# Kernel optimization log

Hardware: AMD Instinct MI355X
Metric: run time of the kernel (lower is better)

## Reference

```python
import jax, jax.numpy as jnp
import numpy as np

N_NODES = 50000
N_EDGES = 200000
IN_FEATS = 32
OUT_FEATS = 32
EDGE_DIM = 16


def setup_inputs() -> dict:
    key = jax.random.key(0)
    k1, k2, k3, k4, k5 = jax.random.split(key, 5)
    feat = jax.random.normal(k1, (N_NODES, IN_FEATS), dtype=jnp.float32)
    efeat = jax.random.normal(k2, (N_EDGES, EDGE_DIM), dtype=jnp.float32)
    src = jax.random.randint(k3, (N_EDGES,), 0, N_NODES, dtype=jnp.int32)
    dst = jax.random.randint(k4, (N_EDGES,), 0, N_NODES, dtype=jnp.int32)
    # edge_func = Linear(EDGE_DIM -> IN_FEATS*OUT_FEATS)
    W_edge = jax.random.normal(k5, (EDGE_DIM, IN_FEATS * OUT_FEATS), dtype=jnp.float32) * (1.0 / np.sqrt(EDGE_DIM))
    b_edge = jnp.zeros((IN_FEATS * OUT_FEATS,), dtype=jnp.float32)
    bias = jnp.zeros((OUT_FEATS,), dtype=jnp.float32)
    return {"feat": feat, "efeat": efeat, "src": src, "dst": dst,
            "W_edge": W_edge, "b_edge": b_edge, "bias": bias}


def reference(feat, efeat, src, dst, W_edge, b_edge, bias):
    # edge_func: (E, edge_dim) -> (E, in, out) edge-conditioned weights
    w = (efeat @ W_edge + b_edge).reshape(-1, IN_FEATS, OUT_FEATS)
    # u_mul_e + sum over in dim  ==  per-edge matvec: h_src[e] @ W[e]
    h_src = feat[src]                               # (E, in) gather
    msg = jnp.einsum('ei,eio->eo', h_src, w)        # (E, out)
    # mean reduce over incoming edges per destination node
    agg = jax.ops.segment_sum(msg, dst, num_segments=N_NODES)   # (N, out)
    deg = jax.ops.segment_sum(jnp.ones((msg.shape[0],), dtype=msg.dtype), dst,
                              num_segments=N_NODES)
    agg = agg / jnp.maximum(deg, 1.0)[:, None]      # zero-degree nodes stay 0
    return agg + bias
```

## Files before the change

kernel.cpp:

```cpp
#include <hip/hip_runtime.h>
#include <hip/hip_bf16.h>

#define NNODES 50000
#define NEDGES 200000
#define WCT_ROW 552
#define WCT_BYTES (32 * WCT_ROW * 2)
#define HROW 40
#define TILE_EDGES 64
#define NTILES (NEDGES / TILE_EDGES)
#define CHAIN_BLKS ((NEDGES + 255) / 256)
#define DROW 36

#define MSG_OFF   0
#define HEAD_OFF  25600000
#define NEXT_OFF  25800000
#define WCT_OFF   26600000

using f32x4 = __attribute__((ext_vector_type(4))) float;
using f16x2 = __attribute__((ext_vector_type(2))) _Float16;
using f16x4 = __attribute__((ext_vector_type(4))) _Float16;
using f16x8 = __attribute__((ext_vector_type(8))) _Float16;

__device__ __forceinline__ f16x2 pkrtz(float a, float b) {
    return __builtin_bit_cast(f16x2, __builtin_amdgcn_cvt_pkrtz(a, b));
}

__device__ __forceinline__ void gload_lds16(const void* g, void* l) {
    __builtin_amdgcn_global_load_lds(
        (const __attribute__((address_space(1))) unsigned int*)g,
        (__attribute__((address_space(3))) unsigned int*)l, 16, 0, 0);
}

#define WCT_BLKS 69
__global__ void init_kernel(const float* __restrict__ W_edge,
                            const float* __restrict__ b_edge,
                            _Float16* __restrict__ wct,
                            unsigned* __restrict__ head) {
    int b = blockIdx.x;
    if (b < WCT_BLKS) {
        int gid = b * 256 + threadIdx.x;
        if (gid >= 32 * WCT_ROW) return;
        int n = gid / WCT_ROW;
        int c = gid - n * WCT_ROW;
        float v = 0.0f;
        if (c < 512)      v = W_edge[(c & 15) * 1024 + (c >> 4) * 32 + n];
        else if (c < 544) v = b_edge[(c - 512) * 32 + n];
        wct[gid] = (_Float16)v;
    } else {
        int gid = (b - WCT_BLKS) * 256 + threadIdx.x;
        if (gid < NNODES) head[gid] = 0xFFFFFFFFu;
    }
}

__global__ __launch_bounds__(256, 3) void work_kernel(
    const float* __restrict__ feat, const float* __restrict__ efeat,
    const int* __restrict__ src, const int* __restrict__ dst,
    const _Float16* __restrict__ wct_g,
    float4* __restrict__ msg4, unsigned* __restrict__ head,
    unsigned* __restrict__ next) {

    __shared__ __align__(16) unsigned short wct_lds[32 * WCT_ROW];
    __shared__ __align__(16) unsigned short h_lds[TILE_EDGES * HROW];
    __shared__ __align__(16) float dtile[TILE_EDGES * DROW];

    const int t = threadIdx.x;

    if (blockIdx.x >= NTILES) {
        int e = (blockIdx.x - NTILES) * 256 + t;
        if (e < NEDGES)
            next[e] = atomicExch(&head[dst[e]], (unsigned)e);
        return;
    }

    const int lane = t & 63;
    const int wave = t >> 6;
    const int ebase = blockIdx.x * TILE_EDGES;

    {
        const char* gsrc = (const char*)wct_g;
        char* lbase = (char*)wct_lds;
        #pragma unroll
        for (int c = 0; c < 9; ++c) {
            int chunk = wave + c * 4;
            if (chunk < 35) {
                int boff = (chunk << 10) + lane * 16;
                if (boff < WCT_BYTES) gload_lds16(gsrc + boff, lbase + boff);
            }
        }
    }

    {
        int et = t >> 2, p = t & 3;
        int se = src[ebase + et];
        const float* fp = feat + se * 32 + p * 8;
        float4 a = *(const float4*)fp;
        float4 b = *(const float4*)(fp + 4);
        uint4 hp;
        hp.x = __builtin_bit_cast(unsigned int, pkrtz(a.x, a.y));
        hp.y = __builtin_bit_cast(unsigned int, pkrtz(a.z, a.w));
        hp.z = __builtin_bit_cast(unsigned int, pkrtz(b.x, b.y));
        hp.w = __builtin_bit_cast(unsigned int, pkrtz(b.z, b.w));
        *(uint4*)(void*)(h_lds + et * HROW + p * 8) = hp;
    }

    const int r16 = lane & 15;
    const int g   = lane >> 4;
    const int wbase = wave * 16;
    const int eg = ebase + wbase + r16;

    const float* efp = efeat + eg * 16 + (g & 1) * 8;
    float4 e0 = *(const float4*)efp;
    float4 e1 = *(const float4*)(efp + 4);
    f16x2 ef2[4] = { pkrtz(e0.x, e0.y), pkrtz(e0.z, e0.w),
                     pkrtz(e1.x, e1.y), pkrtz(e1.z, e1.w) };

    __syncthreads();

    unsigned int hbc[16];
    f16x8 af_bias;
    {
        const uint4* hrow = (const uint4*)(void*)(h_lds + (wbase + r16) * HROW);
        unsigned int hw[16];
        #pragma unroll
        for (int q = 0; q < 4; ++q) {
            uint4 v = hrow[q];
            hw[q*4+0] = v.x; hw[q*4+1] = v.y; hw[q*4+2] = v.z; hw[q*4+3] = v.w;
        }
        const bool hi = (g >> 1) & 1;
        #pragma unroll
        for (int s = 0; s < 16; ++s) {
            unsigned int x = hi ? (hw[s] >> 16) : (hw[s] & 0xffffu);
            hbc[s] = x | (x << 16);
        }
        af_bias = *(const f16x8*)(void*)((const _Float16*)h_lds + (wbase + r16) * HROW + g * 8);
    }

    const _Float16* brow0 = (const _Float16*)wct_lds + r16 * WCT_ROW;
    const _Float16* brow1 = (const _Float16*)wct_lds + (16 + r16) * WCT_ROW;

    f32x4 acc0 = {0.f, 0.f, 0.f, 0.f};
    f32x4 acc1 = {0.f, 0.f, 0.f, 0.f};

    #pragma unroll
    for (int s = 0; s < 16; ++s) {
        const int koff = s * 32 + g * 8;
        f16x8 b0 = *(const f16x8*)(brow0 + koff);
        f16x8 b1 = *(const f16x8*)(brow1 + koff);
        f16x2 hb = __builtin_bit_cast(f16x2, hbc[s]);
        f16x2 p0 = hb * ef2[0], p1 = hb * ef2[1], p2 = hb * ef2[2], p3 = hb * ef2[3];
        f16x4 lo  = __builtin_shufflevector(p0, p1, 0, 1, 2, 3);
        f16x4 hi4 = __builtin_shufflevector(p2, p3, 0, 1, 2, 3);
        f16x8 af  = __builtin_shufflevector(lo, hi4, 0, 1, 2, 3, 4, 5, 6, 7);
        acc0 = __builtin_amdgcn_mfma_f32_16x16x32_f16(af, b0, acc0, 0, 0, 0);
        acc1 = __builtin_amdgcn_mfma_f32_16x16x32_f16(af, b1, acc1, 0, 0, 0);
    }
    {
        const int koff = 512 + g * 8;
        f16x8 b0 = *(const f16x8*)(brow0 + koff);
        f16x8 b1 = *(const f16x8*)(brow1 + koff);
        acc0 = __builtin_amdgcn_mfma_f32_16x16x32_f16(af_bias, b0, acc0, 0, 0, 0);
        acc1 = __builtin_amdgcn_mfma_f32_16x16x32_f16(af_bias, b1, acc1, 0, 0, 0);
    }

    {
        const int browD = wbase + g * 4;
        #pragma unroll
        for (int r = 0; r < 4; ++r) {
            dtile[(browD + r) * DROW + r16]      = acc0[r];
            dtile[(browD + r) * DROW + 16 + r16] = acc1[r];
        }
    }
    __syncthreads();

    {
        const int et = t >> 2, q = t & 3;
        const float* drow = dtile + et * DROW + q * 8;
        float4 v0 = *(const float4*)(drow);
        float4 v1 = *(const float4*)(drow + 4);
        float4* mp = msg4 + (size_t)blockIdx.x * 512;
        mp[t]       = v0;
        mp[256 + t] = v1;
    }
}

__global__ __launch_bounds__(256) void pull_kernel(
    const float4* __restrict__ msg4, const unsigned* __restrict__ head,
    const unsigned* __restrict__ next, const float* __restrict__ bias,
    float* __restrict__ out) {

    int gid = blockIdx.x * 256 + threadIdx.x;
    if (gid >= NNODES * 8) return;
    int n = gid >> 3, Q = gid & 7;

    const unsigned qoff = (unsigned)((Q & 1) * 256 + (Q >> 1));

    float4 s = {0.f, 0.f, 0.f, 0.f};
    float degf = 0.0f;

    unsigned e = head[n];
    while (e != 0xFFFFFFFFu) {
        float4 m = msg4[(size_t)(e >> 6) * 512 + qoff + (e & 63) * 4];
        s.x += m.x; s.y += m.y; s.z += m.z; s.w += m.w;
        degf += 1.0f;
        e = next[e];
    }

    float inv = 1.0f / fmaxf(degf, 1.0f);
    float4 b = ((const float4*)bias)[Q];
    float4 o = { s.x * inv + b.x, s.y * inv + b.y, s.z * inv + b.z, s.w * inv + b.w };
    *(float4*)(out + n * 32 + Q * 4) = o;
}

extern "C" void kernel_launch(void* const* d_in, const int* in_sizes, int n_in,
                              void* d_out, int out_size, void* d_ws, size_t ws_size,
                              hipStream_t stream) {
    const float* feat   = (const float*)d_in[0];
    const float* efeat  = (const float*)d_in[1];
    const int*   src    = (const int*)d_in[2];
    const int*   dst    = (const int*)d_in[3];
    const float* W_edge = (const float*)d_in[4];
    const float* b_edge = (const float*)d_in[5];
    const float* bias   = (const float*)d_in[6];

    char* ws = (char*)d_ws;
    float4*   msg4 = (float4*)(ws + MSG_OFF);
    unsigned* head = (unsigned*)(ws + HEAD_OFF);
    unsigned* next = (unsigned*)(ws + NEXT_OFF);
    _Float16* wct  = (_Float16*)(ws + WCT_OFF);
    float*    out  = (float*)d_out;

    init_kernel<<<WCT_BLKS + (NNODES + 255) / 256, 256, 0, stream>>>(
        W_edge, b_edge, wct, head);
    work_kernel<<<NTILES + CHAIN_BLKS, 256, 0, stream>>>(
        feat, efeat, src, dst, wct, msg4, head, next);
    pull_kernel<<<(NNODES * 8 + 255) / 256, 256, 0, stream>>>(
        msg4, head, next, bias, out);
}
```

Baseline: 46.44 us.

## Read edge-weight matrix from global cache instead of staging in LDS

```diff
diff --git a/kernel.cpp b/kernel.cpp
--- a/kernel.cpp
+++ b/kernel.cpp
@@ -3,8 +3,7 @@
 
 #define NNODES 50000
 #define NEDGES 200000
-#define WCT_ROW 552
-#define WCT_BYTES (32 * WCT_ROW * 2)
+#define WCT_ROW 544
 #define HROW 40
 #define TILE_EDGES 64
 #define NTILES (NEDGES / TILE_EDGES)
@@ -25,13 +24,7 @@
     return __builtin_bit_cast(f16x2, __builtin_amdgcn_cvt_pkrtz(a, b));
 }
 
-__device__ __forceinline__ void gload_lds16(const void* g, void* l) {
-    __builtin_amdgcn_global_load_lds(
-        (const __attribute__((address_space(1))) unsigned int*)g,
-        (__attribute__((address_space(3))) unsigned int*)l, 16, 0, 0);
-}
-
-#define WCT_BLKS 69
+#define WCT_BLKS 68
 __global__ void init_kernel(const float* __restrict__ W_edge,
                             const float* __restrict__ b_edge,
                             _Float16* __restrict__ wct,
@@ -42,9 +35,9 @@
         if (gid >= 32 * WCT_ROW) return;
         int n = gid / WCT_ROW;
         int c = gid - n * WCT_ROW;
-        float v = 0.0f;
-        if (c < 512)      v = W_edge[(c & 15) * 1024 + (c >> 4) * 32 + n];
-        else if (c < 544) v = b_edge[(c - 512) * 32 + n];
+        float v;
+        if (c < 512) v = W_edge[(c & 15) * 1024 + (c >> 4) * 32 + n];
+        else         v = b_edge[(c - 512) * 32 + n];
         wct[gid] = (_Float16)v;
     } else {
         int gid = (b - WCT_BLKS) * 256 + threadIdx.x;
@@ -52,14 +45,13 @@
     }
 }
 
-__global__ __launch_bounds__(256, 3) void work_kernel(
+__global__ __launch_bounds__(256, 6) void work_kernel(
     const float* __restrict__ feat, const float* __restrict__ efeat,
     const int* __restrict__ src, const int* __restrict__ dst,
     const _Float16* __restrict__ wct_g,
     float4* __restrict__ msg4, unsigned* __restrict__ head,
     unsigned* __restrict__ next) {
 
-    __shared__ __align__(16) unsigned short wct_lds[32 * WCT_ROW];
     __shared__ __align__(16) unsigned short h_lds[TILE_EDGES * HROW];
     __shared__ __align__(16) float dtile[TILE_EDGES * DROW];
 
@@ -75,19 +67,6 @@
     const int lane = t & 63;
     const int wave = t >> 6;
     const int ebase = blockIdx.x * TILE_EDGES;
-
-    {
-        const char* gsrc = (const char*)wct_g;
-        char* lbase = (char*)wct_lds;
-        #pragma unroll
-        for (int c = 0; c < 9; ++c) {
-            int chunk = wave + c * 4;
-            if (chunk < 35) {
-                int boff = (chunk << 10) + lane * 16;
-                if (boff < WCT_BYTES) gload_lds16(gsrc + boff, lbase + boff);
-            }
-        }
-    }
 
     {
         int et = t >> 2, p = t & 3;
@@ -114,7 +93,8 @@
     f16x2 ef2[4] = { pkrtz(e0.x, e0.y), pkrtz(e0.z, e0.w),
                      pkrtz(e1.x, e1.y), pkrtz(e1.z, e1.w) };
 
-    __syncthreads();
+    asm volatile("s_waitcnt lgkmcnt(0)" ::: "memory");
+    __builtin_amdgcn_sched_barrier(0);
 
     unsigned int hbc[16];
     f16x8 af_bias;
@@ -135,8 +115,8 @@
         af_bias = *(const f16x8*)(void*)((const _Float16*)h_lds + (wbase + r16) * HROW + g * 8);
     }
 
-    const _Float16* brow0 = (const _Float16*)wct_lds + r16 * WCT_ROW;
-    const _Float16* brow1 = (const _Float16*)wct_lds + (16 + r16) * WCT_ROW;
+    const _Float16* brow0 = wct_g + r16 * WCT_ROW;
+    const _Float16* brow1 = wct_g + (16 + r16) * WCT_ROW;
 
     f32x4 acc0 = {0.f, 0.f, 0.f, 0.f};
     f32x4 acc1 = {0.f, 0.f, 0.f, 0.f};
@@ -170,7 +150,8 @@
             dtile[(browD + r) * DROW + 16 + r16] = acc1[r];
         }
     }
-    __syncthreads();
+    asm volatile("s_waitcnt lgkmcnt(0)" ::: "memory");
+    __builtin_amdgcn_sched_barrier(0);
 
     {
         const int et = t >> 2, q = t & 3;
```

Result: slower. 58.77 us (+26.5%).

## Fuse init, edge compute and pull into one persistent cooperative kernel

Applied to the files above, without the earlier changes.

```diff
diff --git a/kernel.cpp b/kernel.cpp
--- a/kernel.cpp
+++ b/kernel.cpp
@@ -1,5 +1,8 @@
 #include <hip/hip_runtime.h>
 #include <hip/hip_bf16.h>
+#include <hip/hip_cooperative_groups.h>
+
+namespace cg = cooperative_groups;
 
 #define NNODES 50000
 #define NEDGES 200000
@@ -8,8 +11,8 @@
 #define HROW 40
 #define TILE_EDGES 64
 #define NTILES (NEDGES / TILE_EDGES)
-#define CHAIN_BLKS ((NEDGES + 255) / 256)
-#define DROW 36
+#define DROW 33
+#define MAX_GRID 768
 
 #define MSG_OFF   0
 #define HEAD_OFF  25600000
@@ -31,53 +34,45 @@
         (__attribute__((address_space(3))) unsigned int*)l, 16, 0, 0);
 }
 
-#define WCT_BLKS 69
-__global__ void init_kernel(const float* __restrict__ W_edge,
-                            const float* __restrict__ b_edge,
-                            _Float16* __restrict__ wct,
-                            unsigned* __restrict__ head) {
-    int b = blockIdx.x;
-    if (b < WCT_BLKS) {
-        int gid = b * 256 + threadIdx.x;
-        if (gid >= 32 * WCT_ROW) return;
-        int n = gid / WCT_ROW;
-        int c = gid - n * WCT_ROW;
+__global__ __launch_bounds__(256, 3) void fused_kernel(
+    const float* __restrict__ feat, const float* __restrict__ efeat,
+    const int* __restrict__ src, const int* __restrict__ dst,
+    const float* __restrict__ W_edge, const float* __restrict__ b_edge,
+    const float* __restrict__ bias,
+    float4* __restrict__ msg4, unsigned* __restrict__ head,
+    unsigned* __restrict__ next, _Float16* __restrict__ wct,
+    float* __restrict__ out) {
+
+    cg::grid_group grid = cg::this_grid();
+
+    __shared__ __align__(16) unsigned short wct_lds[32 * WCT_ROW];
+    __shared__ __align__(16) unsigned short h_lds[TILE_EDGES * HROW];
+    __shared__ __align__(16) float dtile[TILE_EDGES * DROW];
+
+    const int t = threadIdx.x;
+    const int nb = gridDim.x;
+    const int gtid = blockIdx.x * 256 + t;
+    const int gstride = nb * 256;
+
+    for (int gid = gtid; gid < 32 * WCT_ROW; gid += gstride) {
+        int n = gid / WCT_ROW, c = gid - n * WCT_ROW;
         float v = 0.0f;
         if (c < 512)      v = W_edge[(c & 15) * 1024 + (c >> 4) * 32 + n];
         else if (c < 544) v = b_edge[(c - 512) * 32 + n];
         wct[gid] = (_Float16)v;
-    } else {
-        int gid = (b - WCT_BLKS) * 256 + threadIdx.x;
-        if (gid < NNODES) head[gid] = 0xFFFFFFFFu;
-    }
-}
-
-__global__ __launch_bounds__(256, 3) void work_kernel(
-    const float* __restrict__ feat, const float* __restrict__ efeat,
-    const int* __restrict__ src, const int* __restrict__ dst,
-    const _Float16* __restrict__ wct_g,
-    float4* __restrict__ msg4, unsigned* __restrict__ head,
-    unsigned* __restrict__ next) {
-
-    __shared__ __align__(16) unsigned short wct_lds[32 * WCT_ROW];
-    __shared__ __align__(16) unsigned short h_lds[TILE_EDGES * HROW];
-    __shared__ __align__(16) float dtile[TILE_EDGES * DROW];
-
-    const int t = threadIdx.x;
-
-    if (blockIdx.x >= NTILES) {
-        int e = (blockIdx.x - NTILES) * 256 + t;
-        if (e < NEDGES)
-            next[e] = atomicExch(&head[dst[e]], (unsigned)e);
-        return;
-    }
+    }
+    for (int gid = gtid; gid < NNODES; gid += gstride) head[gid] = 0xFFFFFFFFu;
+
+    grid.sync();
 
     const int lane = t & 63;
     const int wave = t >> 6;
-    const int ebase = blockIdx.x * TILE_EDGES;
+    const int r16  = lane & 15;
+    const int g    = lane >> 4;
+    const int wbase = wave * 16;
 
     {
-        const char* gsrc = (const char*)wct_g;
+        const char* gsrc = (const char*)wct;
         char* lbase = (char*)wct_lds;
         #pragma unroll
         for (int c = 0; c < 9; ++c) {
@@ -88,127 +83,126 @@
             }
         }
     }
-
-    {
-        int et = t >> 2, p = t & 3;
-        int se = src[ebase + et];
-        const float* fp = feat + se * 32 + p * 8;
-        float4 a = *(const float4*)fp;
-        float4 b = *(const float4*)(fp + 4);
-        uint4 hp;
-        hp.x = __builtin_bit_cast(unsigned int, pkrtz(a.x, a.y));
-        hp.y = __builtin_bit_cast(unsigned int, pkrtz(a.z, a.w));
-        hp.z = __builtin_bit_cast(unsigned int, pkrtz(b.x, b.y));
-        hp.w = __builtin_bit_cast(unsigned int, pkrtz(b.z, b.w));
-        *(uint4*)(void*)(h_lds + et * HROW + p * 8) = hp;
-    }
-
-    const int r16 = lane & 15;
-    const int g   = lane >> 4;
-    const int wbase = wave * 16;
-    const int eg = ebase + wbase + r16;
-
-    const float* efp = efeat + eg * 16 + (g & 1) * 8;
-    float4 e0 = *(const float4*)efp;
-    float4 e1 = *(const float4*)(efp + 4);
-    f16x2 ef2[4] = { pkrtz(e0.x, e0.y), pkrtz(e0.z, e0.w),
-                     pkrtz(e1.x, e1.y), pkrtz(e1.z, e1.w) };
-
     __syncthreads();
 
-    unsigned int hbc[16];
-    f16x8 af_bias;
-    {
-        const uint4* hrow = (const uint4*)(void*)(h_lds + (wbase + r16) * HROW);
-        unsigned int hw[16];
-        #pragma unroll
-        for (int q = 0; q < 4; ++q) {
-            uint4 v = hrow[q];
-            hw[q*4+0] = v.x; hw[q*4+1] = v.y; hw[q*4+2] = v.z; hw[q*4+3] = v.w;
-        }
-        const bool hi = (g >> 1) & 1;
+    const _Float16* brow0 = (const _Float16*)wct_lds + r16 * WCT_ROW;
+    const _Float16* brow1 = (const _Float16*)wct_lds + (16 + r16) * WCT_ROW;
+
+    for (int tile = blockIdx.x; tile < NTILES; tile += nb) {
+        const int ebase = tile * TILE_EDGES;
+
+        if (t < TILE_EDGES) {
+            int e = ebase + t;
+            next[e] = atomicExch(&head[dst[e]], (unsigned)e);
+        }
+
+        {
+            int et = t >> 2, p = t & 3;
+            int se = src[ebase + et];
+            const float* fp = feat + se * 32 + p * 8;
+            float4 a = *(const float4*)fp;
+            float4 b = *(const float4*)(fp + 4);
+            uint4 hp;
+            hp.x = __builtin_bit_cast(unsigned int, pkrtz(a.x, a.y));
+            hp.y = __builtin_bit_cast(unsigned int, pkrtz(a.z, a.w));
+            hp.z = __builtin_bit_cast(unsigned int, pkrtz(b.x, b.y));
+            hp.w = __builtin_bit_cast(unsigned int, pkrtz(b.z, b.w));
+            *(uint4*)(void*)(h_lds + et * HROW + p * 8) = hp;
+        }
+
+        const int eg = ebase + wbase + r16;
+        const float* efp = efeat + eg * 16 + (g & 1) * 8;
+        float4 e0 = *(const float4*)efp;
+        float4 e1 = *(const float4*)(efp + 4);
+        f16x2 ef2[4] = { pkrtz(e0.x, e0.y), pkrtz(e0.z, e0.w),
+                         pkrtz(e1.x, e1.y), pkrtz(e1.z, e1.w) };
+
+        asm volatile("s_waitcnt lgkmcnt(0)" ::: "memory");
+        __builtin_amdgcn_sched_barrier(0);
+
+        unsigned int hbc[16];
+        f16x8 af_bias;
+        {
+            const uint4* hrow = (const uint4*)(void*)(h_lds + (wbase + r16) * HROW);
+            unsigned int hw[16];
+            #pragma unroll
+            for (int q = 0; q < 4; ++q) {
+                uint4 v = hrow[q];
+                hw[q*4+0] = v.x; hw[q*4+1] = v.y; hw[q*4+2] = v.z; hw[q*4+3] = v.w;
+            }
+            const bool hi = (g >> 1) & 1;
+            #pragma unroll
+            for (int s = 0; s < 16; ++s) {
+                unsigned int x = hi ? (hw[s] >> 16) : (hw[s] & 0xffffu);
+                hbc[s] = x | (x << 16);
+            }
+            af_bias = *(const f16x8*)(void*)((const _Float16*)h_lds + (wbase + r16) * HROW + g * 8);
+        }
+
+        f32x4 acc0 = {0.f, 0.f, 0.f, 0.f};
+        f32x4 acc1 = {0.f, 0.f, 0.f, 0.f};
+
         #pragma unroll
         for (int s = 0; s < 16; ++s) {
-            unsigned int x = hi ? (hw[s] >> 16) : (hw[s] & 0xffffu);
-            hbc[s] = x | (x << 16);
-        }
-        af_bias = *(const f16x8*)(void*)((const _Float16*)h_lds + (wbase + r16) * HROW + g * 8);
-    }
-
-    const _Float16* brow0 = (const _Float16*)wct_lds + r16 * WCT_ROW;
-    const _Float16* brow1 = (const _Float16*)wct_lds + (16 + r16) * WCT_ROW;
-
-    f32x4 acc0 = {0.f, 0.f, 0.f, 0.f};
-    f32x4 acc1 = {0.f, 0.f, 0.f, 0.f};
-
-    #pragma unroll
-    for (int s = 0; s < 16; ++s) {
-        const int koff = s * 32 + g * 8;
-        f16x8 b0 = *(const f16x8*)(brow0 + koff);
-        f16x8 b1 = *(const f16x8*)(brow1 + koff);
-        f16x2 hb = __builtin_bit_cast(f16x2, hbc[s]);
-        f16x2 p0 = hb * ef2[0], p1 = hb * ef2[1], p2 = hb * ef2[2], p3 = hb * ef2[3];
-        f16x4 lo  = __builtin_shufflevector(p0, p1, 0, 1, 2, 3);
-        f16x4 hi4 = __builtin_shufflevector(p2, p3, 0, 1, 2, 3);
-        f16x8 af  = __builtin_shufflevector(lo, hi4, 0, 1, 2, 3, 4, 5, 6, 7);
-        acc0 = __builtin_amdgcn_mfma_f32_16x16x32_f16(af, b0, acc0, 0, 0, 0);
-        acc1 = __builtin_amdgcn_mfma_f32_16x16x32_f16(af, b1, acc1, 0, 0, 0);
-    }
-    {
-        const int koff = 512 + g * 8;
-        f16x8 b0 = *(const f16x8*)(brow0 + koff);
-        f16x8 b1 = *(const f16x8*)(brow1 + koff);
-        acc0 = __builtin_amdgcn_mfma_f32_16x16x32_f16(af_bias, b0, acc0, 0, 0, 0);
-        acc1 = __builtin_amdgcn_mfma_f32_16x16x32_f16(af_bias, b1, acc1, 0, 0, 0);
-    }
-
-    {
-        const int browD = wbase + g * 4;
-        #pragma unroll
-        for (int r = 0; r < 4; ++r) {
-            dtile[(browD + r) * DROW + r16]      = acc0[r];
-            dtile[(browD + r) * DROW + 16 + r16] = acc1[r];
-        }
-    }
-    __syncthreads();
-
-    {
-        const int et = t >> 2, q = t & 3;
-        const float* drow = dtile + et * DROW + q * 8;
-        float4 v0 = *(const float4*)(drow);
-        float4 v1 = *(const float4*)(drow + 4);
-        float4* mp = msg4 + (size_t)blockIdx.x * 512;
-        mp[t]       = v0;
-        mp[256 + t] = v1;
-    }
-}
-
-__global__ __launch_bounds__(256) void pull_kernel(
-    const float4* __restrict__ msg4, const unsigned* __restrict__ head,
-    const unsigned* __restrict__ next, const float* __restrict__ bias,
-    float* __restrict__ out) {
-
-    int gid = blockIdx.x * 256 + threadIdx.x;
-    if (gid >= NNODES * 8) return;
-    int n = gid >> 3, Q = gid & 7;
-
-    const unsigned qoff = (unsigned)((Q & 1) * 256 + (Q >> 1));
-
-    float4 s = {0.f, 0.f, 0.f, 0.f};
-    float degf = 0.0f;
-
-    unsigned e = head[n];
-    while (e != 0xFFFFFFFFu) {
-        float4 m = msg4[(size_t)(e >> 6) * 512 + qoff + (e & 63) * 4];
-        s.x += m.x; s.y += m.y; s.z += m.z; s.w += m.w;
-        degf += 1.0f;
-        e = next[e];
-    }
-
-    float inv = 1.0f / fmaxf(degf, 1.0f);
-    float4 b = ((const float4*)bias)[Q];
-    float4 o = { s.x * inv + b.x, s.y * inv + b.y, s.z * inv + b.z, s.w * inv + b.w };
-    *(float4*)(out + n * 32 + Q * 4) = o;
+            const int koff = s * 32 + g * 8;
+            f16x8 b0 = *(const f16x8*)(brow0 + koff);
+            f16x8 b1 = *(const f16x8*)(brow1 + koff);
+            f16x2 hb = __builtin_bit_cast(f16x2, hbc[s]);
+            f16x2 p0 = hb * ef2[0], p1 = hb * ef2[1], p2 = hb * ef2[2], p3 = hb * ef2[3];
+            f16x4 lo  = __builtin_shufflevector(p0, p1, 0, 1, 2, 3);
+            f16x4 hi4 = __builtin_shufflevector(p2, p3, 0, 1, 2, 3);
+            f16x8 af  = __builtin_shufflevector(lo, hi4, 0, 1, 2, 3, 4, 5, 6, 7);
+            acc0 = __builtin_amdgcn_mfma_f32_16x16x32_f16(af, b0, acc0, 0, 0, 0);
+            acc1 = __builtin_amdgcn_mfma_f32_16x16x32_f16(af, b1, acc1, 0, 0, 0);
+        }
+        {
+            const int koff = 512 + g * 8;
+            f16x8 b0 = *(const f16x8*)(brow0 + koff);
+            f16x8 b1 = *(const f16x8*)(brow1 + koff);
+            acc0 = __builtin_amdgcn_mfma_f32_16x16x32_f16(af_bias, b0, acc0, 0, 0, 0);
+            acc1 = __builtin_amdgcn_mfma_f32_16x16x32_f16(af_bias, b1, acc1, 0, 0, 0);
+        }
+
+        {
+            const int browD = wbase + g * 4;
+            #pragma unroll
+            for (int r = 0; r < 4; ++r) {
+                dtile[(browD + r) * DROW + r16]      = acc0[r];
+                dtile[(browD + r) * DROW + 16 + r16] = acc1[r];
+            }
+        }
+        asm volatile("s_waitcnt lgkmcnt(0)" ::: "memory");
+        __builtin_amdgcn_sched_barrier(0);
+
+        {
+            const int rA = wbase + (lane >> 3);
+            const int cA = (lane & 7) * 4;
+            float4 vA = *(const float4*)(dtile + rA * DROW + cA);
+            float4 vB = *(const float4*)(dtile + (rA + 8) * DROW + cA);
+            float4* mp = msg4 + (size_t)tile * 512 + wave * 128;
+            mp[lane]      = vA;
+            mp[64 + lane] = vB;
+        }
+    }
+
+    grid.sync();
+
+    for (int gid = gtid; gid < NNODES * 8; gid += gstride) {
+        int n = gid >> 3, Q = gid & 7;
+        float4 s = {0.f, 0.f, 0.f, 0.f};
+        float degf = 0.0f;
+        unsigned e = head[n];
+        while (e != 0xFFFFFFFFu) {
+            float4 m = msg4[(size_t)e * 8 + Q];
+            s.x += m.x; s.y += m.y; s.z += m.z; s.w += m.w;
+            degf += 1.0f;
+            e = next[e];
+        }
+        float inv = 1.0f / fmaxf(degf, 1.0f);
+        float4 b = ((const float4*)bias)[Q];
+        float4 o = { s.x * inv + b.x, s.y * inv + b.y, s.z * inv + b.z, s.w * inv + b.w };
+        *(float4*)(out + n * 32 + Q * 4) = o;
+    }
 }
 
 extern "C" void kernel_launch(void* const* d_in, const int* in_sizes, int n_in,
@@ -229,10 +223,16 @@
     _Float16* wct  = (_Float16*)(ws + WCT_OFF);
     float*    out  = (float*)d_out;
 
-    init_kernel<<<WCT_BLKS + (NNODES + 255) / 256, 256, 0, stream>>>(
-        W_edge, b_edge, wct, head);
-    work_kernel<<<NTILES + CHAIN_BLKS, 256, 0, stream>>>(
-        feat, efeat, src, dst, wct, msg4, head, next);
-    pull_kernel<<<(NNODES * 8 + 255) / 256, 256, 0, stream>>>(
-        msg4, head, next, bias, out);
-}
+    int maxb = 0;
+    (void)hipOccupancyMaxActiveBlocksPerMultiprocessor(&maxb, fused_kernel, 256, 0);
+    if (maxb < 1) maxb = 1;
+    int grid = maxb * 256;
+    if (grid > MAX_GRID) grid = MAX_GRID;
+
+    void* args[] = { (void*)&feat, (void*)&efeat, (void*)&src, (void*)&dst,
+                     (void*)&W_edge, (void*)&b_edge, (void*)&bias,
+                     (void*)&msg4, (void*)&head, (void*)&next, (void*)&wct,
+                     (void*)&out };
+    (void)hipLaunchCooperativeKernel((void*)fused_kernel, dim3(grid), dim3(256),
+                                     args, 0, stream);
+}
```

Result: slower. 182.3 us (+292.5%).
